# Optimization experiments

Measured on AMD Instinct MI355X. Metric: run time of the kernel, lower is better.

## Reference

```python
import jax, jax.numpy as jnp
import numpy as np

B, S, D = 2, 2048, 1024
H = 16
HD = D // H  # 64
EPS = 1e-6
ROPE_BASE = 10000.0


def _rms_norm(x, w, eps=EPS):
    # torch nn.RMSNorm over last dim
    var = jnp.mean(jnp.square(x), axis=-1, keepdims=True)
    return x * jax.lax.rsqrt(var + eps) * w


def _rope_tables(seq_len, head_dim, base=ROPE_BASE):
    inv_freq = 1.0 / (base ** (jnp.arange(0, head_dim, 2, dtype=jnp.float32) / head_dim))
    t = jnp.arange(seq_len, dtype=jnp.float32)
    freqs = t[:, None] * inv_freq[None, :]            # [S, HD/2]
    emb = jnp.concatenate([freqs, freqs], axis=-1)    # [S, HD]
    return jnp.cos(emb), jnp.sin(emb)


def _rotate_half(x):
    x1, x2 = jnp.split(x, 2, axis=-1)
    return jnp.concatenate([-x2, x1], axis=-1)


def _apply_rope(x, cos, sin):
    # x: [B, H, S, HD]; cos/sin: [S, HD]
    return x * cos[None, None] + _rotate_half(x) * sin[None, None]


def setup_inputs() -> dict:
    key = jax.random.key(0)
    ks = jax.random.split(key, 8)
    scale = 1.0 / np.sqrt(D)
    return {
        "x": jax.random.normal(ks[0], (B, S, D), dtype=jnp.float32),
        "wq": jax.random.normal(ks[1], (D, D), dtype=jnp.float32) * scale,
        "wk": jax.random.normal(ks[2], (D, D), dtype=jnp.float32) * scale,
        "wv": jax.random.normal(ks[3], (D, D), dtype=jnp.float32) * scale,
        "wo": jax.random.normal(ks[4], (D, D), dtype=jnp.float32) * scale,
        "q_norm_w": jnp.ones((HD,), dtype=jnp.float32),
        "k_norm_w": jnp.ones((HD,), dtype=jnp.float32),
        "sink_logit": jnp.zeros((H,), dtype=jnp.float32),
    }


def reference(x, wq, wk, wv, wo, q_norm_w, k_norm_w, sink_logit):
    b, s, _ = x.shape
    # QKV projections (nn.Linear, no bias): y = x @ W^T
    q = jnp.einsum("bsd,od->bso", x, wq).reshape(b, s, H, HD)
    k = jnp.einsum("bsd,od->bso", x, wk).reshape(b, s, H, HD)
    v = jnp.einsum("bsd,od->bso", x, wv).reshape(b, s, H, HD)
    # QK RMSNorm (per head_dim)
    q = _rms_norm(q, q_norm_w)
    k = _rms_norm(k, k_norm_w)
    # [B, H, S, HD]
    q = q.transpose(0, 2, 1, 3)
    k = k.transpose(0, 2, 1, 3)
    v = v.transpose(0, 2, 1, 3)
    # full-head RoPE
    cos, sin = _rope_tables(s, HD)
    q = _apply_rope(q, cos, sin)
    k = _apply_rope(k, cos, sin)
    # manual attention with causal mask and sink softmax
    scale = HD ** -0.5
    scores = jnp.einsum("bhqd,bhkd->bhqk", q, k) * scale  # [B,H,S,S]
    causal = jnp.tril(jnp.ones((s, s), dtype=bool))
    scores = jnp.where(causal[None, None], scores, -jnp.inf)
    # sink-augmented softmax in fp32: append per-head sink logit, softmax, drop sink column
    sink = jnp.broadcast_to(sink_logit.astype(jnp.float32)[None, :, None, None], (b, H, s, 1))
    aug = jnp.concatenate([scores.astype(jnp.float32), sink], axis=-1)
    weights = jax.nn.softmax(aug, axis=-1)[..., :s].astype(scores.dtype)
    out = jnp.einsum("bhqk,bhkd->bhqd", weights, v)
    out = out.transpose(0, 2, 1, 3).reshape(b, s, D)
    return jnp.einsum("bsd,od->bso", out, wo)
```

## Files before the change

### kernel.cpp

```cpp
#include <hip/hip_runtime.h>

#define Bb 2
#define Ss 2048
#define Dd 1024
#define Hh 16
#define HDd 64
#define BS (Bb * Ss)

typedef __attribute__((ext_vector_type(8))) __bf16 bf16x8;
typedef __attribute__((ext_vector_type(8))) unsigned short u16x8;
typedef __attribute__((ext_vector_type(4))) float f32x4;

__device__ __forceinline__ unsigned short f2bf(float f) {
  union { float f; unsigned u; } v; v.f = f;
  unsigned r = v.u + 0x7fffu + ((v.u >> 16) & 1u);
  return (unsigned short)(r >> 16);
}
__device__ __forceinline__ unsigned short f2bf_fast(float f) {
  union { float f; unsigned u; } v; v.f = f;
  return (unsigned short)((v.u + 0x8000u) >> 16);
}

__device__ __forceinline__ void gl_lds16(const void* g, void* l) {
  __builtin_amdgcn_global_load_lds(
      (const __attribute__((address_space(1))) void*)g,
      (__attribute__((address_space(3))) void*)l, 16, 0, 0);
}

__global__ __launch_bounds__(256) void cast_all(
    const float4* __restrict__ x, const float4* __restrict__ wq,
    const float4* __restrict__ wk, const float4* __restrict__ wv,
    const float4* __restrict__ wo, ushort4* __restrict__ xb,
    ushort4* __restrict__ wqkvb, ushort4* __restrict__ wob,
    float* __restrict__ ct, float* __restrict__ st) {
  int i = blockIdx.x * 256 + threadIdx.x;
  const int NX4 = BS * Dd / 4;
  const int NW4 = Dd * Dd / 4;
  const float4* src;
  ushort4* dst;
  int idx;
  if (i < NX4) { src = x; dst = xb; idx = i; }
  else if ((i -= NX4) < NW4) { src = wq; dst = wqkvb; idx = i; }
  else if ((i -= NW4) < NW4) { src = wk; dst = wqkvb + NW4; idx = i; }
  else if ((i -= NW4) < NW4) { src = wv; dst = wqkvb + 2 * NW4; idx = i; }
  else if ((i -= NW4) < NW4) { src = wo; dst = wob; idx = i; }
  else if ((i -= NW4) < Ss * 32) {
    int s = i >> 5, jj = i & 31;
    float freq = __powf(10000.0f, -(float)jj * (1.0f / 32.0f));
    float cs, sn;
    sincosf((float)s * freq, &sn, &cs);
    ct[i] = cs; st[i] = sn;
    return;
  } else return;
  float4 v = src[idx];
  ushort4 o;
  o.x = f2bf(v.x); o.y = f2bf(v.y); o.z = f2bf(v.z); o.w = f2bf(v.w);
  dst[idx] = o;
}

__global__ __launch_bounds__(256, 3) void gemm_qkv(
    const unsigned short* __restrict__ A, const unsigned short* __restrict__ Bw,
    const float* __restrict__ qw, const float* __restrict__ kw,
    const float* __restrict__ ct, const float* __restrict__ st,
    unsigned short* __restrict__ Qb, unsigned short* __restrict__ Kb,
    unsigned short* __restrict__ Vt) {
  __shared__ __align__(16) unsigned short As[128 * 32];
  __shared__ __align__(16) unsigned short Bs[128 * 32];
  const int K = Dd, tid = threadIdx.x;
  const int lane = tid & 63;
  const int quad = lane >> 4;
  const int l16 = lane & 15;
  const int wave = tid >> 6;
  const int wm = (wave >> 1) * 64;
  const int wn = (wave & 1) * 64;
  const int tile_m = blockIdx.y * 128;
  const int tile_n = blockIdx.x * 128;

  const int off0 = tid * 16;
  const int off1 = 4096 + tid * 16;
  const int r0 = tid >> 2, r1 = r0 + 64;
  const int sch = (((tid & 3) ^ ((tid >> 3) & 3)) << 3);
  const int xg = ((quad ^ ((l16 >> 1) & 3)) << 3);

  const unsigned short* Ag0 = A + (size_t)(tile_m + r0) * K + sch;
  const unsigned short* Ag1 = A + (size_t)(tile_m + r1) * K + sch;
  const unsigned short* Bg0 = Bw + (size_t)(tile_n + r0) * K + sch;
  const unsigned short* Bg1 = Bw + (size_t)(tile_n + r1) * K + sch;

  f32x4 zero = {0.f, 0.f, 0.f, 0.f};
  f32x4 acc[4][4];
#pragma unroll
  for (int mi = 0; mi < 4; ++mi)
#pragma unroll
    for (int ni = 0; ni < 4; ++ni) acc[mi][ni] = zero;

  for (int k0 = 0; k0 < K; k0 += 32) {
    gl_lds16(Ag0 + k0, (char*)As + off0);
    gl_lds16(Ag1 + k0, (char*)As + off1);
    gl_lds16(Bg0 + k0, (char*)Bs + off0);
    gl_lds16(Bg1 + k0, (char*)Bs + off1);
    __syncthreads();
    bf16x8 af[4], bfv[4];
#pragma unroll
    for (int mi = 0; mi < 4; ++mi)
      af[mi] = *(const bf16x8*)&As[(wm + mi * 16 + l16) * 32 + xg];
#pragma unroll
    for (int ni = 0; ni < 4; ++ni)
      bfv[ni] = *(const bf16x8*)&Bs[(wn + ni * 16 + l16) * 32 + xg];
#pragma unroll
    for (int mi = 0; mi < 4; ++mi)
#pragma unroll
      for (int ni = 0; ni < 4; ++ni)
        acc[mi][ni] = __builtin_amdgcn_mfma_f32_16x16x32_bf16(
            af[mi], bfv[ni], acc[mi][ni], 0, 0, 0);
    __syncthreads();
  }

  const int type = blockIdx.x >> 3;
  const int h = (((blockIdx.x & 7) << 7) + wn) >> 6;
  const int bb = tile_m >> 11;
  const size_t bh = (size_t)bb * Hh + h;

  if (type == 2) {
#pragma unroll
    for (int mi = 0; mi < 4; ++mi) {
      int s0 = (tile_m + wm + mi * 16 + quad * 4) & (Ss - 1);
#pragma unroll
      for (int ni = 0; ni < 4; ++ni) {
        int d = ni * 16 + l16;
        ushort4 pv;
        pv.x = f2bf(acc[mi][ni][0]);
        pv.y = f2bf(acc[mi][ni][1]);
        pv.z = f2bf(acc[mi][ni][2]);
        pv.w = f2bf(acc[mi][ni][3]);
        *(ushort4*)&Vt[(bh * HDd + d) * Ss + s0] = pv;
      }
    }
  } else {
    const float* wnp = type ? kw : qw;
    unsigned short* Ob = type ? Kb : Qb;
    const float fscale = type ? 1.0f : 0.125f * 1.44269504f;
    float w0[4];
#pragma unroll
    for (int ni = 0; ni < 4; ++ni) w0[ni] = wnp[ni * 16 + l16];
#pragma unroll
    for (int mi = 0; mi < 4; ++mi) {
#pragma unroll
      for (int r = 0; r < 4; ++r) {
        int s = (tile_m + wm + mi * 16 + quad * 4 + r) & (Ss - 1);
        float ss2 = 0.f;
#pragma unroll
        for (int ni = 0; ni < 4; ++ni) ss2 += acc[mi][ni][r] * acc[mi][ni][r];
        ss2 += __shfl_xor(ss2, 1, 64);
        ss2 += __shfl_xor(ss2, 2, 64);
        ss2 += __shfl_xor(ss2, 4, 64);
        ss2 += __shfl_xor(ss2, 8, 64);
        float rr = rsqrtf(ss2 * (1.0f / 64.0f) + 1e-6f) * fscale;
        float c0 = ct[s * 32 + l16], c1 = ct[s * 32 + 16 + l16];
        float sn0 = st[s * 32 + l16], sn1 = st[s * 32 + 16 + l16];
#pragma unroll
        for (int ni = 0; ni < 4; ++ni) {
          float vn = acc[mi][ni][r] * rr * w0[ni];
          float vp = acc[mi][ni ^ 2][r] * rr * w0[ni ^ 2];
          float cs_ = (ni & 1) ? c1 : c0;
          float sn_ = (ni & 1) ? sn1 : sn0;
          float sg = (ni < 2) ? -1.0f : 1.0f;
          Ob[(bh * Ss + s) * HDd + ni * 16 + l16] = f2bf(vn * cs_ + sg * vp * sn_);
        }
      }
    }
  }
}

__global__ __launch_bounds__(256) void gemm_bt2(
    const unsigned short* __restrict__ A, const unsigned short* __restrict__ Bw,
    float* __restrict__ C, int M, int N, int K) {
  __shared__ __align__(16) unsigned short As[128 * 32];
  __shared__ __align__(16) unsigned short Bs[64 * 32];
  const int tid = threadIdx.x;
  const int lane = tid & 63;
  const int quad = lane >> 4;
  const int l16 = lane & 15;
  const int wave = tid >> 6;
  const int wm = (wave >> 1) * 64;
  const int wn = (wave & 1) * 32;
  const int tile_m = blockIdx.y * 128;
  const int tile_n = blockIdx.x * 64;

  const int off0 = tid * 16;
  const int off1 = 4096 + tid * 16;
  const int r0 = tid >> 2, r1 = r0 + 64;
  const int sch = (((tid & 3) ^ ((tid >> 3) & 3)) << 3);
  const int xg = ((quad ^ ((l16 >> 1) & 3)) << 3);

  const unsigned short* Ag0 = A + (size_t)(tile_m + r0) * K + sch;
  const unsigned short* Ag1 = A + (size_t)(tile_m + r1) * K + sch;
  const unsigned short* Bg0 = Bw + (size_t)(tile_n + r0) * K + sch;

  f32x4 zero = {0.f, 0.f, 0.f, 0.f};
  f32x4 acc[4][2];
#pragma unroll
  for (int mi = 0; mi < 4; ++mi)
#pragma unroll
    for (int ni = 0; ni < 2; ++ni) acc[mi][ni] = zero;

  for (int k0 = 0; k0 < K; k0 += 32) {
    gl_lds16(Ag0 + k0, (char*)As + off0);
    gl_lds16(Ag1 + k0, (char*)As + off1);
    gl_lds16(Bg0 + k0, (char*)Bs + off0);
    __syncthreads();
    bf16x8 af[4], bfv[2];
#pragma unroll
    for (int mi = 0; mi < 4; ++mi)
      af[mi] = *(const bf16x8*)&As[(wm + mi * 16 + l16) * 32 + xg];
#pragma unroll
    for (int ni = 0; ni < 2; ++ni)
      bfv[ni] = *(const bf16x8*)&Bs[(wn + ni * 16 + l16) * 32 + xg];
#pragma unroll
    for (int mi = 0; mi < 4; ++mi)
#pragma unroll
      for (int ni = 0; ni < 2; ++ni)
        acc[mi][ni] = __builtin_amdgcn_mfma_f32_16x16x32_bf16(
            af[mi], bfv[ni], acc[mi][ni], 0, 0, 0);
    __syncthreads();
  }

#pragma unroll
  for (int mi = 0; mi < 4; ++mi) {
#pragma unroll
    for (int ni = 0; ni < 2; ++ni) {
      int col = tile_n + wn + ni * 16 + l16;
#pragma unroll
      for (int r = 0; r < 4; ++r) {
        int row = tile_m + wm + mi * 16 + quad * 4 + r;
        C[(size_t)row * N + col] = acc[mi][ni][r];
      }
    }
  }
}

__global__ __launch_bounds__(256, 4) void flash(
    const unsigned short* __restrict__ Qb, const unsigned short* __restrict__ Kb,
    const unsigned short* __restrict__ Vt, const float* __restrict__ sink,
    unsigned short* __restrict__ Ob) {
  __shared__ __align__(16) unsigned short Ks[2][64 * 64];
  __shared__ __align__(16) unsigned short Vs[2][64 * 64];
  __shared__ __align__(16) unsigned short Ps[4][16 * 64];

  int tid = threadIdx.x, lane = tid & 63, wave = tid >> 6;
  int quad = lane >> 4, l16 = lane & 15;

  int lid = blockIdx.x;
  int g = lid >> 8, j = lid & 255;
  int hb = j >> 3, t = j & 7;
  int b = hb >> 4, h = hb & 15;
  int qt = (g == 0) ? t : (g == 1) ? 31 - t : (g == 2) ? 8 + t : 23 - t;

  const unsigned short* Qg = Qb + ((size_t)(b * Hh + h) * Ss) * HDd;
  const unsigned short* Kg = Kb + ((size_t)(b * Hh + h) * Ss) * HDd;
  const unsigned short* Vg = Vt + ((size_t)(b * Hh + h) * HDd) * Ss;

  int off0 = tid * 16, off1 = 4096 + tid * 16;
  int sr0 = tid >> 3, sr1 = sr0 + 32;
  int sch = ((tid & 7) ^ (sr0 & 7)) * 8;
  int x0 = ((quad ^ (l16 & 7)) * 8);
  int x1 = x0 ^ 32;

  int q0 = qt * 64;
  int myq = q0 + wave * 16 + l16;

  float sk = sink[h];
  f32x4 zero = {0.f, 0.f, 0.f, 0.f};

  bf16x8 ones;
  {
    u16x8 tt;
#pragma unroll
    for (int i = 0; i < 8; ++i) tt[i] = 0x3F80;
    ones = *(bf16x8*)&tt;
  }

  const unsigned short* Qrow = Qg + (size_t)myq * HDd;
  bf16x8 aq0 = *(const bf16x8*)(Qrow + quad * 8);
  bf16x8 aq1 = *(const bf16x8*)(Qrow + 32 + quad * 8);

  gl_lds16(Kg + (size_t)sr0 * 64 + sch, (char*)Ks[0] + off0);
  gl_lds16(Kg + (size_t)sr1 * 64 + sch, (char*)Ks[0] + off1);
  gl_lds16(Vg + (size_t)sr0 * Ss + sch, (char*)Vs[0] + off0);
  gl_lds16(Vg + (size_t)sr1 * Ss + sch, (char*)Vs[0] + off1);

  f32x4 Oacc[4], lacc = zero;
#pragma unroll
  for (int ni = 0; ni < 4; ++ni) Oacc[ni] = zero;

  __syncthreads();
  if (qt >= 1) {
    gl_lds16(Kg + (size_t)(64 + sr0) * 64 + sch, (char*)Ks[1] + off0);
    gl_lds16(Kg + (size_t)(64 + sr1) * 64 + sch, (char*)Ks[1] + off1);
  }

  f32x4 sc[4];
#pragma unroll
  for (int ni = 0; ni < 4; ++ni) {
    bf16x8 bk0 = *(const bf16x8*)&Ks[0][(ni * 16 + l16) * 64 + x0];
    bf16x8 bk1 = *(const bf16x8*)&Ks[0][(ni * 16 + l16) * 64 + x1];
    sc[ni] = __builtin_amdgcn_mfma_f32_16x16x32_bf16(bk0, aq0, zero, 0, 0, 0);
    sc[ni] = __builtin_amdgcn_mfma_f32_16x16x32_bf16(bk1, aq1, sc[ni], 0, 0, 0);
  }
  if (qt == 0) {
#pragma unroll
    for (int ni = 0; ni < 4; ++ni)
#pragma unroll
      for (int r = 0; r < 4; ++r)
        if (ni * 16 + quad * 4 + r > myq - q0) sc[ni][r] = -1.0e38f;
  }

  char* Pw = (char*)Ps[wave];
  const int prow = l16 * 128;
  const int psw = l16 & 7;

  for (int kt = 0; kt <= qt; ++kt) {
    bool last = (kt == qt);
    if (qt > 0) __syncthreads();
    if (kt + 2 <= qt) {
      gl_lds16(Kg + (size_t)((kt + 2) * 64 + sr0) * 64 + sch, (char*)Ks[kt & 1] + off0);
      gl_lds16(Kg + (size_t)((kt + 2) * 64 + sr1) * 64 + sch, (char*)Ks[kt & 1] + off1);
    }
    if (kt + 1 <= qt) {
      gl_lds16(Vg + (size_t)sr0 * Ss + (kt + 1) * 64 + sch, (char*)Vs[(kt + 1) & 1] + off0);
      gl_lds16(Vg + (size_t)sr1 * Ss + (kt + 1) * 64 + sch, (char*)Vs[(kt + 1) & 1] + off1);
    }

#pragma unroll
    for (int ni = 0; ni < 4; ++ni) {
      ushort4 pk;
      pk.x = f2bf_fast(exp2f(sc[ni][0]));
      pk.y = f2bf_fast(exp2f(sc[ni][1]));
      pk.z = f2bf_fast(exp2f(sc[ni][2]));
      pk.w = f2bf_fast(exp2f(sc[ni][3]));
      int chunk = (ni * 2 + (quad >> 1)) ^ psw;
      *(ushort4*)(Pw + prow + chunk * 16 + (quad & 1) * 8) = pk;
    }

    f32x4 scn[4];
    if (!last) {
      const unsigned short* Kt = Ks[(kt + 1) & 1];
#pragma unroll
      for (int ni = 0; ni < 4; ++ni) {
        bf16x8 bk0 = *(const bf16x8*)&Kt[(ni * 16 + l16) * 64 + x0];
        bf16x8 bk1 = *(const bf16x8*)&Kt[(ni * 16 + l16) * 64 + x1];
        scn[ni] = __builtin_amdgcn_mfma_f32_16x16x32_bf16(bk0, aq0, zero, 0, 0, 0);
        scn[ni] = __builtin_amdgcn_mfma_f32_16x16x32_bf16(bk1, aq1, scn[ni], 0, 0, 0);
      }
      if (kt + 1 == qt) {
#pragma unroll
        for (int ni = 0; ni < 4; ++ni)
#pragma unroll
          for (int r = 0; r < 4; ++r)
            if ((kt + 1) * 64 + ni * 16 + quad * 4 + r > myq) scn[ni][r] = -1.0e38f;
      }
    }

    asm volatile("s_waitcnt lgkmcnt(0)" ::: "memory");
    bf16x8 ap0 = *(const bf16x8*)(Pw + prow + ((quad ^ psw) * 16));
    bf16x8 ap1 = *(const bf16x8*)(Pw + prow + (((quad + 4) ^ psw) * 16));

    const unsigned short* Vtile = Vs[kt & 1];
#pragma unroll
    for (int ni = 0; ni < 4; ++ni) {
      bf16x8 bv0 = *(const bf16x8*)&Vtile[(ni * 16 + l16) * 64 + x0];
      bf16x8 bv1 = *(const bf16x8*)&Vtile[(ni * 16 + l16) * 64 + x1];
      Oacc[ni] = __builtin_amdgcn_mfma_f32_16x16x32_bf16(bv0, ap0, Oacc[ni], 0, 0, 0);
      Oacc[ni] = __builtin_amdgcn_mfma_f32_16x16x32_bf16(bv1, ap1, Oacc[ni], 0, 0, 0);
    }
    lacc = __builtin_amdgcn_mfma_f32_16x16x32_bf16(ones, ap0, lacc, 0, 0, 0);
    lacc = __builtin_amdgcn_mfma_f32_16x16x32_bf16(ones, ap1, lacc, 0, 0, 0);

    if (!last) {
#pragma unroll
      for (int ni = 0; ni < 4; ++ni) sc[ni] = scn[ni];
    }
  }

  float inv = 1.0f / (lacc[0] + exp2f(sk * 1.44269504f));
#pragma unroll
  for (int ni = 0; ni < 4; ++ni) {
    ushort4 ov;
    ov.x = f2bf(Oacc[ni][0] * inv);
    ov.y = f2bf(Oacc[ni][1] * inv);
    ov.z = f2bf(Oacc[ni][2] * inv);
    ov.w = f2bf(Oacc[ni][3] * inv);
    *(ushort4*)&Ob[((size_t)b * Ss + myq) * Dd + h * 64 + ni * 16 + quad * 4] = ov;
  }
}

extern "C" void kernel_launch(void* const* d_in, const int* in_sizes, int n_in,
                              void* d_out, int out_size, void* d_ws, size_t ws_size,
                              hipStream_t stream) {
  const float* x  = (const float*)d_in[0];
  const float* wq = (const float*)d_in[1];
  const float* wk = (const float*)d_in[2];
  const float* wv = (const float*)d_in[3];
  const float* wo = (const float*)d_in[4];
  const float* qw = (const float*)d_in[5];
  const float* kw = (const float*)d_in[6];
  const float* sk = (const float*)d_in[7];

  char* ws = (char*)d_ws;
  const size_t MB = 1ull << 20;
  unsigned short* xb    = (unsigned short*)(ws + 0);
  unsigned short* attnb = (unsigned short*)(ws + 0);
  unsigned short* wqkvb = (unsigned short*)(ws + 8 * MB);
  unsigned short* wob   = (unsigned short*)(ws + 14 * MB);
  float*          ct    = (float*)(ws + 16 * MB);
  float*          st    = (float*)(ws + 17 * MB);
  unsigned short* Qb    = (unsigned short*)(ws + 40 * MB);
  unsigned short* Kb    = (unsigned short*)(ws + 48 * MB);
  unsigned short* Vt    = (unsigned short*)(ws + 56 * MB);

  cast_all<<<8448, 256, 0, stream>>>(
      (const float4*)x, (const float4*)wq, (const float4*)wk, (const float4*)wv,
      (const float4*)wo, (ushort4*)xb, (ushort4*)wqkvb, (ushort4*)wob, ct, st);
  gemm_qkv<<<dim3(24, 32), 256, 0, stream>>>(xb, wqkvb, qw, kw, ct, st, Qb, Kb, Vt);
  flash<<<dim3(1024), 256, 0, stream>>>(Qb, Kb, Vt, sk, attnb);
  gemm_bt2<<<dim3(16, 32), 256, 0, stream>>>(attnb, wob, (float*)d_out, BS, Dd, Dd);
}
```

Measured before the change: 182.7 us.

## Pair causal query tiles per block to share K/V tiles and balance work

Each flash block now handles two query tiles (t and 31-t) of the same head, so every block does the same total number of K/V iterations and each loaded K/V tile serves both query tiles. The grid halves to 512 blocks and launch bounds drop to 2 blocks per SM, since registers roughly double for the second set of accumulators. This is meant to cut redundant K/V loads and fix load imbalance across blocks, at the cost of lower occupancy and fewer blocks to fill the CUs.

```diff
diff --git a/kernel.cpp b/kernel.cpp
--- a/kernel.cpp
+++ b/kernel.cpp
@@ -239,22 +239,22 @@
   }
 }
 
-__global__ __launch_bounds__(256, 4) void flash(
+__global__ __launch_bounds__(256, 2) void flash(
     const unsigned short* __restrict__ Qb, const unsigned short* __restrict__ Kb,
     const unsigned short* __restrict__ Vt, const float* __restrict__ sink,
     unsigned short* __restrict__ Ob) {
   __shared__ __align__(16) unsigned short Ks[2][64 * 64];
   __shared__ __align__(16) unsigned short Vs[2][64 * 64];
-  __shared__ __align__(16) unsigned short Ps[4][16 * 64];
+  __shared__ __align__(16) unsigned short Ps[2][4][16 * 64];
 
   int tid = threadIdx.x, lane = tid & 63, wave = tid >> 6;
   int quad = lane >> 4, l16 = lane & 15;
 
   int lid = blockIdx.x;
-  int g = lid >> 8, j = lid & 255;
-  int hb = j >> 3, t = j & 7;
-  int b = hb >> 4, h = hb & 15;
-  int qt = (g == 0) ? t : (g == 1) ? 31 - t : (g == 2) ? 8 + t : 23 - t;
+  int h = (lid & 7) + 8 * ((lid >> 3) & 1);
+  int t = (lid >> 4) & 15;
+  int b = lid >> 8;
+  const int qta = t, qtb = 31 - t;
 
   const unsigned short* Qg = Qb + ((size_t)(b * Hh + h) * Ss) * HDd;
   const unsigned short* Kg = Kb + ((size_t)(b * Hh + h) * Ss) * HDd;
@@ -266,8 +266,8 @@
   int x0 = ((quad ^ (l16 & 7)) * 8);
   int x1 = x0 ^ 32;
 
-  int q0 = qt * 64;
-  int myq = q0 + wave * 16 + l16;
+  int myqa = qta * 64 + wave * 16 + l16;
+  int myqb = qtb * 64 + wave * 16 + l16;
 
   float sk = sink[h];
   f32x4 zero = {0.f, 0.f, 0.f, 0.f};
@@ -280,53 +280,58 @@
     ones = *(bf16x8*)&tt;
   }
 
-  const unsigned short* Qrow = Qg + (size_t)myq * HDd;
-  bf16x8 aq0 = *(const bf16x8*)(Qrow + quad * 8);
-  bf16x8 aq1 = *(const bf16x8*)(Qrow + 32 + quad * 8);
+  const unsigned short* Qra = Qg + (size_t)myqa * HDd;
+  const unsigned short* Qrb = Qg + (size_t)myqb * HDd;
+  bf16x8 aq0a = *(const bf16x8*)(Qra + quad * 8);
+  bf16x8 aq1a = *(const bf16x8*)(Qra + 32 + quad * 8);
+  bf16x8 aq0b = *(const bf16x8*)(Qrb + quad * 8);
+  bf16x8 aq1b = *(const bf16x8*)(Qrb + 32 + quad * 8);
 
   gl_lds16(Kg + (size_t)sr0 * 64 + sch, (char*)Ks[0] + off0);
   gl_lds16(Kg + (size_t)sr1 * 64 + sch, (char*)Ks[0] + off1);
   gl_lds16(Vg + (size_t)sr0 * Ss + sch, (char*)Vs[0] + off0);
   gl_lds16(Vg + (size_t)sr1 * Ss + sch, (char*)Vs[0] + off1);
 
-  f32x4 Oacc[4], lacc = zero;
-#pragma unroll
-  for (int ni = 0; ni < 4; ++ni) Oacc[ni] = zero;
+  f32x4 Oacca[4], Oaccb[4], lacca = zero, laccb = zero;
+#pragma unroll
+  for (int ni = 0; ni < 4; ++ni) { Oacca[ni] = zero; Oaccb[ni] = zero; }
 
   __syncthreads();
-  if (qt >= 1) {
-    gl_lds16(Kg + (size_t)(64 + sr0) * 64 + sch, (char*)Ks[1] + off0);
-    gl_lds16(Kg + (size_t)(64 + sr1) * 64 + sch, (char*)Ks[1] + off1);
-  }
-
-  f32x4 sc[4];
+  gl_lds16(Kg + (size_t)(64 + sr0) * 64 + sch, (char*)Ks[1] + off0);
+  gl_lds16(Kg + (size_t)(64 + sr1) * 64 + sch, (char*)Ks[1] + off1);
+
+  f32x4 sca[4], scb[4];
 #pragma unroll
   for (int ni = 0; ni < 4; ++ni) {
     bf16x8 bk0 = *(const bf16x8*)&Ks[0][(ni * 16 + l16) * 64 + x0];
     bf16x8 bk1 = *(const bf16x8*)&Ks[0][(ni * 16 + l16) * 64 + x1];
-    sc[ni] = __builtin_amdgcn_mfma_f32_16x16x32_bf16(bk0, aq0, zero, 0, 0, 0);
-    sc[ni] = __builtin_amdgcn_mfma_f32_16x16x32_bf16(bk1, aq1, sc[ni], 0, 0, 0);
-  }
-  if (qt == 0) {
+    scb[ni] = __builtin_amdgcn_mfma_f32_16x16x32_bf16(bk0, aq0b, zero, 0, 0, 0);
+    scb[ni] = __builtin_amdgcn_mfma_f32_16x16x32_bf16(bk1, aq1b, scb[ni], 0, 0, 0);
+    sca[ni] = __builtin_amdgcn_mfma_f32_16x16x32_bf16(bk0, aq0a, zero, 0, 0, 0);
+    sca[ni] = __builtin_amdgcn_mfma_f32_16x16x32_bf16(bk1, aq1a, sca[ni], 0, 0, 0);
+  }
+  if (qta == 0) {
 #pragma unroll
     for (int ni = 0; ni < 4; ++ni)
 #pragma unroll
       for (int r = 0; r < 4; ++r)
-        if (ni * 16 + quad * 4 + r > myq - q0) sc[ni][r] = -1.0e38f;
-  }
-
-  char* Pw = (char*)Ps[wave];
+        if (ni * 16 + quad * 4 + r > myqa) sca[ni][r] = -1.0e38f;
+  }
+
+  char* Pwa = (char*)Ps[0][wave];
+  char* Pwb = (char*)Ps[1][wave];
   const int prow = l16 * 128;
   const int psw = l16 & 7;
 
-  for (int kt = 0; kt <= qt; ++kt) {
-    bool last = (kt == qt);
-    if (qt > 0) __syncthreads();
-    if (kt + 2 <= qt) {
+  for (int kt = 0; kt <= qtb; ++kt) {
+    bool last = (kt == qtb);
+    bool acta = (kt <= qta);
+    __syncthreads();
+    if (kt + 2 <= qtb) {
       gl_lds16(Kg + (size_t)((kt + 2) * 64 + sr0) * 64 + sch, (char*)Ks[kt & 1] + off0);
       gl_lds16(Kg + (size_t)((kt + 2) * 64 + sr1) * 64 + sch, (char*)Ks[kt & 1] + off1);
     }
-    if (kt + 1 <= qt) {
+    if (kt + 1 <= qtb) {
       gl_lds16(Vg + (size_t)sr0 * Ss + (kt + 1) * 64 + sch, (char*)Vs[(kt + 1) & 1] + off0);
       gl_lds16(Vg + (size_t)sr1 * Ss + (kt + 1) * 64 + sch, (char*)Vs[(kt + 1) & 1] + off1);
     }
@@ -334,63 +339,112 @@
 #pragma unroll
     for (int ni = 0; ni < 4; ++ni) {
       ushort4 pk;
-      pk.x = f2bf_fast(exp2f(sc[ni][0]));
-      pk.y = f2bf_fast(exp2f(sc[ni][1]));
-      pk.z = f2bf_fast(exp2f(sc[ni][2]));
-      pk.w = f2bf_fast(exp2f(sc[ni][3]));
+      pk.x = f2bf_fast(exp2f(scb[ni][0]));
+      pk.y = f2bf_fast(exp2f(scb[ni][1]));
+      pk.z = f2bf_fast(exp2f(scb[ni][2]));
+      pk.w = f2bf_fast(exp2f(scb[ni][3]));
       int chunk = (ni * 2 + (quad >> 1)) ^ psw;
-      *(ushort4*)(Pw + prow + chunk * 16 + (quad & 1) * 8) = pk;
-    }
-
-    f32x4 scn[4];
+      *(ushort4*)(Pwb + prow + chunk * 16 + (quad & 1) * 8) = pk;
+    }
+    if (acta) {
+#pragma unroll
+      for (int ni = 0; ni < 4; ++ni) {
+        ushort4 pk;
+        pk.x = f2bf_fast(exp2f(sca[ni][0]));
+        pk.y = f2bf_fast(exp2f(sca[ni][1]));
+        pk.z = f2bf_fast(exp2f(sca[ni][2]));
+        pk.w = f2bf_fast(exp2f(sca[ni][3]));
+        int chunk = (ni * 2 + (quad >> 1)) ^ psw;
+        *(ushort4*)(Pwa + prow + chunk * 16 + (quad & 1) * 8) = pk;
+      }
+    }
+
+    f32x4 scnb[4], scna[4];
     if (!last) {
       const unsigned short* Kt = Ks[(kt + 1) & 1];
 #pragma unroll
       for (int ni = 0; ni < 4; ++ni) {
         bf16x8 bk0 = *(const bf16x8*)&Kt[(ni * 16 + l16) * 64 + x0];
         bf16x8 bk1 = *(const bf16x8*)&Kt[(ni * 16 + l16) * 64 + x1];
-        scn[ni] = __builtin_amdgcn_mfma_f32_16x16x32_bf16(bk0, aq0, zero, 0, 0, 0);
-        scn[ni] = __builtin_amdgcn_mfma_f32_16x16x32_bf16(bk1, aq1, scn[ni], 0, 0, 0);
-      }
-      if (kt + 1 == qt) {
+        scnb[ni] = __builtin_amdgcn_mfma_f32_16x16x32_bf16(bk0, aq0b, zero, 0, 0, 0);
+        scnb[ni] = __builtin_amdgcn_mfma_f32_16x16x32_bf16(bk1, aq1b, scnb[ni], 0, 0, 0);
+        if (kt + 1 <= qta) {
+          scna[ni] = __builtin_amdgcn_mfma_f32_16x16x32_bf16(bk0, aq0a, zero, 0, 0, 0);
+          scna[ni] = __builtin_amdgcn_mfma_f32_16x16x32_bf16(bk1, aq1a, scna[ni], 0, 0, 0);
+        }
+      }
+      if (kt + 1 == qtb) {
 #pragma unroll
         for (int ni = 0; ni < 4; ++ni)
 #pragma unroll
           for (int r = 0; r < 4; ++r)
-            if ((kt + 1) * 64 + ni * 16 + quad * 4 + r > myq) scn[ni][r] = -1.0e38f;
+            if ((kt + 1) * 64 + ni * 16 + quad * 4 + r > myqb) scnb[ni][r] = -1.0e38f;
+      }
+      if (kt + 1 == qta) {
+#pragma unroll
+        for (int ni = 0; ni < 4; ++ni)
+#pragma unroll
+          for (int r = 0; r < 4; ++r)
+            if ((kt + 1) * 64 + ni * 16 + quad * 4 + r > myqa) scna[ni][r] = -1.0e38f;
       }
     }
 
     asm volatile("s_waitcnt lgkmcnt(0)" ::: "memory");
-    bf16x8 ap0 = *(const bf16x8*)(Pw + prow + ((quad ^ psw) * 16));
-    bf16x8 ap1 = *(const bf16x8*)(Pw + prow + (((quad + 4) ^ psw) * 16));
+    bf16x8 ap0b = *(const bf16x8*)(Pwb + prow + ((quad ^ psw) * 16));
+    bf16x8 ap1b = *(const bf16x8*)(Pwb + prow + (((quad + 4) ^ psw) * 16));
 
     const unsigned short* Vtile = Vs[kt & 1];
 #pragma unroll
     for (int ni = 0; ni < 4; ++ni) {
       bf16x8 bv0 = *(const bf16x8*)&Vtile[(ni * 16 + l16) * 64 + x0];
       bf16x8 bv1 = *(const bf16x8*)&Vtile[(ni * 16 + l16) * 64 + x1];
-      Oacc[ni] = __builtin_amdgcn_mfma_f32_16x16x32_bf16(bv0, ap0, Oacc[ni], 0, 0, 0);
-      Oacc[ni] = __builtin_amdgcn_mfma_f32_16x16x32_bf16(bv1, ap1, Oacc[ni], 0, 0, 0);
-    }
-    lacc = __builtin_amdgcn_mfma_f32_16x16x32_bf16(ones, ap0, lacc, 0, 0, 0);
-    lacc = __builtin_amdgcn_mfma_f32_16x16x32_bf16(ones, ap1, lacc, 0, 0, 0);
+      Oaccb[ni] = __builtin_amdgcn_mfma_f32_16x16x32_bf16(bv0, ap0b, Oaccb[ni], 0, 0, 0);
+      Oaccb[ni] = __builtin_amdgcn_mfma_f32_16x16x32_bf16(bv1, ap1b, Oaccb[ni], 0, 0, 0);
+    }
+    laccb = __builtin_amdgcn_mfma_f32_16x16x32_bf16(ones, ap0b, laccb, 0, 0, 0);
+    laccb = __builtin_amdgcn_mfma_f32_16x16x32_bf16(ones, ap1b, laccb, 0, 0, 0);
+
+    if (acta) {
+      bf16x8 ap0a = *(const bf16x8*)(Pwa + prow + ((quad ^ psw) * 16));
+      bf16x8 ap1a = *(const bf16x8*)(Pwa + prow + (((quad + 4) ^ psw) * 16));
+#pragma unroll
+      for (int ni = 0; ni < 4; ++ni) {
+        bf16x8 bv0 = *(const bf16x8*)&Vtile[(ni * 16 + l16) * 64 + x0];
+        bf16x8 bv1 = *(const bf16x8*)&Vtile[(ni * 16 + l16) * 64 + x1];
+        Oacca[ni] = __builtin_amdgcn_mfma_f32_16x16x32_bf16(bv0, ap0a, Oacca[ni], 0, 0, 0);
+        Oacca[ni] = __builtin_amdgcn_mfma_f32_16x16x32_bf16(bv1, ap1a, Oacca[ni], 0, 0, 0);
+      }
+      lacca = __builtin_amdgcn_mfma_f32_16x16x32_bf16(ones, ap0a, lacca, 0, 0, 0);
+      lacca = __builtin_amdgcn_mfma_f32_16x16x32_bf16(ones, ap1a, lacca, 0, 0, 0);
+    }
 
     if (!last) {
 #pragma unroll
-      for (int ni = 0; ni < 4; ++ni) sc[ni] = scn[ni];
-    }
-  }
-
-  float inv = 1.0f / (lacc[0] + exp2f(sk * 1.44269504f));
+      for (int ni = 0; ni < 4; ++ni) scb[ni] = scnb[ni];
+      if (kt + 1 <= qta) {
+#pragma unroll
+        for (int ni = 0; ni < 4; ++ni) sca[ni] = scna[ni];
+      }
+    }
+  }
+
+  float sinkw = exp2f(sk * 1.44269504f);
+  float inva = 1.0f / (lacca[0] + sinkw);
+  float invb = 1.0f / (laccb[0] + sinkw);
 #pragma unroll
   for (int ni = 0; ni < 4; ++ni) {
     ushort4 ov;
-    ov.x = f2bf(Oacc[ni][0] * inv);
-    ov.y = f2bf(Oacc[ni][1] * inv);
-    ov.z = f2bf(Oacc[ni][2] * inv);
-    ov.w = f2bf(Oacc[ni][3] * inv);
-    *(ushort4*)&Ob[((size_t)b * Ss + myq) * Dd + h * 64 + ni * 16 + quad * 4] = ov;
+    ov.x = f2bf(Oacca[ni][0] * inva);
+    ov.y = f2bf(Oacca[ni][1] * inva);
+    ov.z = f2bf(Oacca[ni][2] * inva);
+    ov.w = f2bf(Oacca[ni][3] * inva);
+    *(ushort4*)&Ob[((size_t)b * Ss + myqa) * Dd + h * 64 + ni * 16 + quad * 4] = ov;
+    ushort4 ow;
+    ow.x = f2bf(Oaccb[ni][0] * invb);
+    ow.y = f2bf(Oaccb[ni][1] * invb);
+    ow.z = f2bf(Oaccb[ni][2] * invb);
+    ow.w = f2bf(Oaccb[ni][3] * invb);
+    *(ushort4*)&Ob[((size_t)b * Ss + myqb) * Dd + h * 64 + ni * 16 + quad * 4] = ow;
   }
 }
 
@@ -422,6 +476,6 @@
       (const float4*)x, (const float4*)wq, (const float4*)wk, (const float4*)wv,
       (const float4*)wo, (ushort4*)xb, (ushort4*)wqkvb, (ushort4*)wob, ct, st);
   gemm_qkv<<<dim3(24, 32), 256, 0, stream>>>(xb, wqkvb, qw, kw, ct, st, Qb, Kb, Vt);
-  flash<<<dim3(1024), 256, 0, stream>>>(Qb, Kb, Vt, sk, attnb);
+  flash<<<dim3(512), 256, 0, stream>>>(Qb, Kb, Vt, sk, attnb);
   gemm_bt2<<<dim3(16, 32), 256, 0, stream>>>(attnb, wob, (float*)d_out, BS, Dd, Dd);
 }
```

Measured after the change: 190.6 us. 1.04x slower.
